# Kernel optimization log

Measured on AMD Instinct MI355X. Metric: run time of the kernel, lower is better.

Reference implementation:

```python
import jax, jax.numpy as jnp
import numpy as np

N, E, F, H, G = 50000, 600000, 128, 128, 256
EPS = 1e-5
NEG_SLOPE = 0.2


def setup_inputs() -> dict:
    key = jax.random.key(0)
    ks = jax.random.split(key, 20)
    def w(k, shape, fan_in):
        return jax.random.normal(k, shape, jnp.float32) / np.sqrt(fan_in)
    x = jax.random.normal(ks[0], (N, F), jnp.float32)
    edge_index = jax.random.randint(ks[1], (2, E), 0, N, jnp.int32)
    batch = jnp.sort(jax.random.randint(ks[2], (N,), 0, G, jnp.int32))
    return {
        "x": x, "edge_index": edge_index, "batch": batch,
        "W1": w(ks[3], (F, H), F), "b1": jnp.zeros((H,), jnp.float32),
        "g1": jnp.ones((H,), jnp.float32), "be1": jnp.zeros((H,), jnp.float32),
        "Wg": w(ks[4], (H, H), H), "att_src": w(ks[5], (H,), H),
        "att_dst": w(ks[6], (H,), H), "bg": jnp.zeros((H,), jnp.float32),
        "g2": jnp.ones((H,), jnp.float32), "be2": jnp.zeros((H,), jnp.float32),
        "W3": w(ks[7], (H, H), H), "b3": jnp.zeros((H,), jnp.float32),
        "g3": jnp.ones((H,), jnp.float32), "be3": jnp.zeros((H,), jnp.float32),
        "fw1": w(ks[8], (H, H), H), "fb1": jnp.zeros((H,), jnp.float32),
        "fw2": w(ks[9], (H, 1), H), "fb2": jnp.zeros((1,), jnp.float32),
    }


def _with_self_loops(edge_index):
    loop = jnp.arange(N, dtype=edge_index.dtype)
    src = jnp.concatenate([edge_index[0], loop])
    dst = jnp.concatenate([edge_index[1], loop])
    return src, dst


def gcn_conv(x, W, b, src, dst):
    h = x @ W                                      # [N,H]
    deg = jax.ops.segment_sum(jnp.ones_like(dst, jnp.float32), dst, num_segments=N)
    dis = jnp.where(deg > 0, jax.lax.rsqrt(jnp.maximum(deg, 1.0)), 0.0)
    norm = dis[src] * dis[dst]                     # [E+N]
    msg = h[src] * norm[:, None]
    return jax.ops.segment_sum(msg, dst, num_segments=N) + b


def gat_conv(x, W, a_src, a_dst, b, src, dst):
    # single-head PyG GATConv with self loops
    h = x @ W                                      # [N,H]
    al_s = h @ a_src                               # [N]
    al_d = h @ a_dst
    e = jax.nn.leaky_relu(al_s[src] + al_d[dst], NEG_SLOPE)   # [E+N]
    m = jax.ops.segment_max(e, dst, num_segments=N)
    ex = jnp.exp(e - m[dst])
    denom = jax.ops.segment_sum(ex, dst, num_segments=N)
    alpha = ex / denom[dst]
    out = jax.ops.segment_sum(h[src] * alpha[:, None], dst, num_segments=N)
    return out + b


def batch_norm(x, gamma, beta):
    mu = jnp.mean(x, axis=0)
    var = jnp.var(x, axis=0)
    return gamma * (x - mu) * jax.lax.rsqrt(var + EPS) + beta


def reference(x, edge_index, batch, W1, b1, g1, be1, Wg, att_src, att_dst, bg,
              g2, be2, W3, b3, g3, be3, fw1, fb1, fw2, fb2):
    src, dst = _with_self_loops(edge_index)
    h = jax.nn.relu(batch_norm(gcn_conv(x, W1, b1, src, dst), g1, be1))
    # dropout = identity (eval mode)
    h = jax.nn.relu(batch_norm(gat_conv(h, Wg, att_src, att_dst, bg, src, dst), g2, be2))
    h = jax.nn.relu(batch_norm(gcn_conv(h, W3, b3, src, dst), g3, be3))
    # global mean pool over graphs
    sums = jax.ops.segment_sum(h, batch, num_segments=G)           # [G,H]
    cnts = jax.ops.segment_sum(jnp.ones((h.shape[0],), h.dtype), batch, num_segments=G)
    pooled = sums / jnp.maximum(cnts, 1.0)[:, None]
    z = jax.nn.relu(pooled @ fw1 + fb1)
    return z @ fw2 + fb2                                            # [G,1]
```

## Files before the change

### kernel.cpp

```cpp
#include <hip/hip_runtime.h>
#include <hip/hip_fp16.h>
#include <cstdint>

#define N_NODES 50000
#define N_EDGES 600000
#define HDIM    128
#define NGRAPH  256
#define EPSBN   1e-5f
#define NEG     0.2f
#define SCAN_B  196

__device__ __forceinline__ float lrelu(float v){ return v > 0.f ? v : NEG*v; }

typedef _Float16 f16x8 __attribute__((ext_vector_type(8)));
typedef float    f32x4 __attribute__((ext_vector_type(4)));

__global__ void prep_kernel(const float* __restrict__ W1, const float* __restrict__ Wg,
                            const float* __restrict__ W3, __half* __restrict__ Wt1,
                            __half* __restrict__ Wtg, __half* __restrict__ Wt3,
                            const int* __restrict__ ei, int* __restrict__ degi,
                            const int* __restrict__ batch, int* __restrict__ start){
  int b = blockIdx.x;
  if (b < 192){
    const float* W = (b < 64) ? W1 : (b < 128 ? Wg : W3);
    __half*     Wt = (b < 64) ? Wt1 : (b < 128 ? Wtg : Wt3);
    int idx = (b & 63)*256 + threadIdx.x;
    int k = idx >> 7, n = idx & 127;
    Wt[n*128 + k] = __float2half(W[idx]);
  } else if (b < 192 + 2344){
    int e = (b - 192)*256 + threadIdx.x;
    if (e < N_EDGES) atomicAdd(&degi[ei[N_EDGES + e]], 1);
  } else {
    int i = (b - 192 - 2344)*256 + threadIdx.x;
    if (i >= N_NODES) return;
    int bb = batch[i];
    int p = (i == 0) ? -1 : batch[i-1];
    for (int g = p+1; g <= bb; ++g) start[g] = i;
    if (i == N_NODES-1)
      for (int g = bb+1; g <= NGRAPH; ++g) start[g] = N_NODES;
  }
}

template<bool BN, bool F32IN, bool ATT, bool SCALE>
__global__ __launch_bounds__(256) void gemm_mfma(const void* __restrict__ Xv,
    const __half* __restrict__ Wt, const __half* __restrict__ scH,
    const __half* __restrict__ shH, __half* __restrict__ Yh,
    const float* __restrict__ asr, const float* __restrict__ adt,
    float* __restrict__ al_s, float* __restrict__ al_d,
    const float* __restrict__ dis){
  const int t    = threadIdx.x;
  const int wave = t >> 6, lane = t & 63;
  const int q    = lane >> 4, c16 = lane & 15;
  const int m0   = blockIdx.x*64 + wave*16;
  const int row  = m0 + c16;
  const int arow = (row > N_NODES-1) ? N_NODES-1 : row;

  f32x4 acc[8];
#pragma unroll
  for (int i = 0; i < 8; ++i) acc[i] = (f32x4){0.f,0.f,0.f,0.f};

  const f16x8* Wt8 = (const f16x8*)Wt;

#pragma unroll
  for (int kc = 0; kc < 4; ++kc){
    const int kof = kc*32 + q*8;
    f16x8 a;
    if (F32IN){
      const float* xp = (const float*)Xv + (long)arow*128 + kof;
      float4 x0 = *(const float4*)xp;
      float4 x1 = *(const float4*)(xp + 4);
      a[0]=(_Float16)x0.x; a[1]=(_Float16)x0.y; a[2]=(_Float16)x0.z; a[3]=(_Float16)x0.w;
      a[4]=(_Float16)x1.x; a[5]=(_Float16)x1.y; a[6]=(_Float16)x1.z; a[7]=(_Float16)x1.w;
    } else {
      f16x8 raw = *(const f16x8*)((const _Float16*)Xv + (long)arow*128 + kof);
      if (BN){
        f16x8 scv = *(const f16x8*)((const _Float16*)scH + kof);
        f16x8 shv = *(const f16x8*)((const _Float16*)shH + kof);
#pragma unroll
        for (int i = 0; i < 8; ++i){
          _Float16 v = (_Float16)(raw[i]*scv[i] + shv[i]);
          a[i] = v > (_Float16)0 ? v : (_Float16)0;
        }
      } else {
        a = raw;
      }
    }
#pragma unroll
    for (int nt = 0; nt < 8; ++nt){
      f16x8 b = Wt8[(nt*16 + c16)*16 + kc*4 + q];
      acc[nt] = __builtin_amdgcn_mfma_f32_16x16x32_f16(b, a, acc[nt], 0, 0, 0);
    }
  }
  float rs = SCALE ? dis[arow] : 1.f;
  if (row < N_NODES){
    __half* yp = Yh + (long)row*128 + q*4;
#pragma unroll
    for (int nt = 0; nt < 8; ++nt){
      union { uint2 u; __half2 h[2]; } pk;
      pk.h[0] = __floats2half2_rn(acc[nt][0]*rs, acc[nt][1]*rs);
      pk.h[1] = __floats2half2_rn(acc[nt][2]*rs, acc[nt][3]*rs);
      *(uint2*)(yp + nt*16) = pk.u;
    }
  }
  if (ATT){
    float s = 0.f, d = 0.f;
#pragma unroll
    for (int nt = 0; nt < 8; ++nt){
      float4 av = *(const float4*)(asr + nt*16 + q*4);
      float4 bv = *(const float4*)(adt + nt*16 + q*4);
      s += acc[nt][0]*av.x + acc[nt][1]*av.y + acc[nt][2]*av.z + acc[nt][3]*av.w;
      d += acc[nt][0]*bv.x + acc[nt][1]*bv.y + acc[nt][2]*bv.z + acc[nt][3]*bv.w;
    }
    s += __shfl_xor(s, 16); s += __shfl_xor(s, 32);
    d += __shfl_xor(d, 16); d += __shfl_xor(d, 32);
    if (q == 0 && row < N_NODES){ al_s[row] = s; al_d[row] = d; }
  }
}

__global__ void scan_partial(const int* __restrict__ degi, int* __restrict__ part,
                             float* __restrict__ dis){
  __shared__ int sm[256];
  int t = threadIdx.x; int i = blockIdx.x*256 + t;
  int v = (i < N_NODES) ? degi[i] : 0;
  if (i < N_NODES) dis[i] = rsqrtf((float)v + 1.f);
  sm[t] = v;
  __syncthreads();
  for (int off = 128; off; off >>= 1){
    if (t < off) sm[t] += sm[t + off];
    __syncthreads();
  }
  if (t == 0) part[blockIdx.x] = sm[0];
}
__global__ void scan_offsets(int* part){
  __shared__ int sm[256];
  int t = threadIdx.x;
  int v = (t < SCAN_B) ? part[t] : 0;
  sm[t] = v; __syncthreads();
  for (int off = 1; off < 256; off <<= 1){
    int add = (t >= off) ? sm[t - off] : 0;
    __syncthreads();
    sm[t] += add; __syncthreads();
  }
  if (t < SCAN_B) part[t] = sm[t] - v;
}
__global__ void scan_final(const int* __restrict__ degi, const int* __restrict__ part,
                           int* __restrict__ rowp){
  __shared__ int sm[256];
  int t = threadIdx.x; int i = blockIdx.x*256 + t;
  int v = (i < N_NODES) ? degi[i] : 0;
  sm[t] = v; __syncthreads();
  for (int off = 1; off < 256; off <<= 1){
    int add = (t >= off) ? sm[t - off] : 0;
    __syncthreads();
    sm[t] += add; __syncthreads();
  }
  if (i < N_NODES) rowp[i] = part[blockIdx.x] + sm[t] - v;
}
__global__ void csr_scatter(const int* __restrict__ ei, const int* __restrict__ rowp,
                            int* __restrict__ fill, int* __restrict__ colx){
  int e = blockIdx.x*256 + threadIdx.x;
  if (e >= N_EDGES) return;
  int s = ei[e], d = ei[N_EDGES + e];
  int pos = rowp[d] + atomicAdd(&fill[d], 1);
  colx[pos] = s;
}

__global__ __launch_bounds__(256) void gcn_agg(const _Float16* __restrict__ Ah,
    const float* __restrict__ dis, const int* __restrict__ rowp,
    const int* __restrict__ degi, const int* __restrict__ colx,
    __half* __restrict__ Bh){
  const int n = blockIdx.x*4 + (threadIdx.x >> 6);
  const int lane = threadIdx.x & 63;
  const int g = lane >> 4, p = lane & 15;
  float acc[8] = {0,0,0,0,0,0,0,0};
  if (g == 0){
    f16x8 self = *(const f16x8*)(Ah + (long)n*128 + p*8);
#pragma unroll
    for (int i = 0; i < 8; ++i) acc[i] = (float)self[i];
  }
  const int e0 = rowp[n], cnt = degi[n];
  for (int base = 0; base < cnt; base += 64){
    int idx = base + lane;
    int s = 0; float w = 0.f;
    if (idx < cnt){ s = colx[e0 + idx]; w = 1.f; }
    int nit = min(64, cnt - base);
    int j = 0;
    for (; j + 8 <= nit; j += 8){
      int   s0 = __shfl(s, j + g),      s1 = __shfl(s, j + 4 + g);
      float w0 = __shfl(w, j + g),      w1 = __shfl(w, j + 4 + g);
      f16x8 r0 = *(const f16x8*)(Ah + (long)s0*128 + p*8);
      f16x8 r1 = *(const f16x8*)(Ah + (long)s1*128 + p*8);
#pragma unroll
      for (int i = 0; i < 8; ++i) acc[i] += w0 * (float)r0[i];
#pragma unroll
      for (int i = 0; i < 8; ++i) acc[i] += w1 * (float)r1[i];
    }
    for (; j < nit; j += 4){
      int   sj = __shfl(s, j + g);
      float wj = __shfl(w, j + g);
      f16x8 r = *(const f16x8*)(Ah + (long)sj*128 + p*8);
#pragma unroll
      for (int i = 0; i < 8; ++i) acc[i] += wj * (float)r[i];
    }
  }
#pragma unroll
  for (int i = 0; i < 8; ++i){
    acc[i] += __shfl_xor(acc[i], 16);
    acc[i] += __shfl_xor(acc[i], 32);
  }
  if (g == 0){
    float dn = dis[n];
    union { uint4 u; __half2 h[4]; } pk;
#pragma unroll
    for (int i = 0; i < 4; ++i)
      pk.h[i] = __floats2half2_rn(acc[2*i]*dn, acc[2*i+1]*dn);
    *(uint4*)(Bh + (long)n*128 + p*8) = pk.u;
  }
}

__global__ __launch_bounds__(256) void gat_agg(const _Float16* __restrict__ Ah,
    const float* __restrict__ al_s, const float* __restrict__ al_d,
    const int* __restrict__ rowp, const int* __restrict__ degi,
    const int* __restrict__ colx, __half* __restrict__ Bh){
  const int n = blockIdx.x*4 + (threadIdx.x >> 6);
  const int lane = threadIdx.x & 63;
  const int g = lane >> 4, p = lane & 15;
  const float adn = al_d[n];
  const float lself = lrelu(al_s[n] + adn);
  const int e0 = rowp[n], cnt = degi[n];
  int sReg = 0; float lv = -1e30f;
  if (lane < cnt){ sReg = colx[e0 + lane]; lv = lrelu(al_s[sReg] + adn); }
  float m = fmaxf(lself, lv);
  for (int base = 64; base < cnt; base += 64){
    int idx = base + lane;
    if (idx < cnt) m = fmaxf(m, lrelu(al_s[colx[e0 + idx]] + adn));
  }
#pragma unroll
  for (int off = 32; off; off >>= 1) m = fmaxf(m, __shfl_xor(m, off));
  const float exs = __expf(lself - m);
  float w = __expf(lv - m);
  float dpart = w;
  float acc[8] = {0,0,0,0,0,0,0,0};
  if (g == 0){
    f16x8 self = *(const f16x8*)(Ah + (long)n*128 + p*8);
#pragma unroll
    for (int i = 0; i < 8; ++i) acc[i] = exs * (float)self[i];
  }
  {
    int nit = min(64, cnt);
    int j = 0;
    for (; j + 8 <= nit; j += 8){
      int   s0 = __shfl(sReg, j + g),   s1 = __shfl(sReg, j + 4 + g);
      float w0 = __shfl(w,    j + g),   w1 = __shfl(w,    j + 4 + g);
      f16x8 r0 = *(const f16x8*)(Ah + (long)s0*128 + p*8);
      f16x8 r1 = *(const f16x8*)(Ah + (long)s1*128 + p*8);
#pragma unroll
      for (int i = 0; i < 8; ++i) acc[i] += w0 * (float)r0[i];
#pragma unroll
      for (int i = 0; i < 8; ++i) acc[i] += w1 * (float)r1[i];
    }
    for (; j < nit; j += 4){
      int   sj = __shfl(sReg, j + g);
      float wj = __shfl(w,    j + g);
      f16x8 r = *(const f16x8*)(Ah + (long)sj*128 + p*8);
#pragma unroll
      for (int i = 0; i < 8; ++i) acc[i] += wj * (float)r[i];
    }
  }
  for (int base = 64; base < cnt; base += 64){
    int idx = base + lane;
    int s2 = 0; float w2 = 0.f;
    if (idx < cnt){ s2 = colx[e0 + idx]; w2 = __expf(lrelu(al_s[s2] + adn) - m); }
    dpart += w2;
    int nit = min(64, cnt - base);
    for (int j = 0; j < nit; j += 4){
      int   sj = __shfl(s2, j + g);
      float wj = __shfl(w2, j + g);
      f16x8 r = *(const f16x8*)(Ah + (long)sj*128 + p*8);
#pragma unroll
      for (int i = 0; i < 8; ++i) acc[i] += wj * (float)r[i];
    }
  }
#pragma unroll
  for (int off = 32; off; off >>= 1) dpart += __shfl_xor(dpart, off);
#pragma unroll
  for (int i = 0; i < 8; ++i){
    acc[i] += __shfl_xor(acc[i], 16);
    acc[i] += __shfl_xor(acc[i], 32);
  }
  if (g == 0){
    float rinv = 1.f / (dpart + exs);
    union { uint4 u; __half2 h[4]; } pk;
#pragma unroll
    for (int i = 0; i < 4; ++i)
      pk.h[i] = __floats2half2_rn(acc[2*i]*rinv, acc[2*i+1]*rinv);
    *(uint4*)(Bh + (long)n*128 + p*8) = pk.u;
  }
}

__global__ void stats_h(const __half2* __restrict__ X2,
                        float* __restrict__ S, float* __restrict__ Q){
  __shared__ float s0m[256], s1m[256], q0m[256], q1m[256];
  int t = threadIdx.x;
  float s0=0,s1=0,q0=0,q1=0;
  int stride = gridDim.x*256;
  const int total = N_NODES*64;
  for (int idx = blockIdx.x*256 + t; idx < total; idx += stride){
    float2 f = __half22float2(X2[idx]);
    s0 += f.x; q0 += f.x*f.x; s1 += f.y; q1 += f.y*f.y;
  }
  s0m[t]=s0; s1m[t]=s1; q0m[t]=q0; q1m[t]=q1;
  __syncthreads();
  if (t < 64){
    float a0 = s0m[t]+s0m[t+64]+s0m[t+128]+s0m[t+192];
    float a1 = s1m[t]+s1m[t+64]+s1m[t+128]+s1m[t+192];
    float b0 = q0m[t]+q0m[t+64]+q0m[t+128]+q0m[t+192];
    float b1 = q1m[t]+q1m[t+64]+q1m[t+128]+q1m[t+192];
    atomicAdd(&S[2*t],   a0); atomicAdd(&S[2*t+1], a1);
    atomicAdd(&Q[2*t],   b0); atomicAdd(&Q[2*t+1], b1);
  }
}
__global__ void bnparam(const float* __restrict__ S, const float* __restrict__ Q,
                        const float* __restrict__ g, const float* __restrict__ be,
                        float* __restrict__ sc, float* __restrict__ sh,
                        __half* __restrict__ scH, __half* __restrict__ shH){
  int c = threadIdx.x;
  float mean = S[c] / (float)N_NODES;
  float var  = fmaxf(Q[c]/(float)N_NODES - mean*mean, 0.f);
  float scale = g[c]*rsqrtf(var + EPSBN);
  float shift = be[c] - mean*scale;
  sc[c] = scale;  sh[c] = shift;
  scH[c] = __float2half(scale);
  shH[c] = __float2half(shift);
}

__global__ void pool_h(const __half* __restrict__ Bh, const int* __restrict__ start,
                       const float* __restrict__ sc, const float* __restrict__ sh,
                       float* __restrict__ Pq){
  int g = blockIdx.x >> 2, q = blockIdx.x & 3, f = threadIdx.x;
  int s0 = start[g], len = start[g+1] - s0;
  int n0 = s0 + (len*q)/4, n1 = s0 + (len*(q+1))/4;
  float scl = sc[f], shf = sh[f];
  float acc = 0.f;
  for (int n = n0; n < n1; ++n)
    acc += fmaxf(__half2float(Bh[(long)n*128 + f])*scl + shf, 0.f);
  Pq[(long)blockIdx.x*128 + f] = acc;
}

__global__ void final_kernel(const float* __restrict__ Pq, const int* __restrict__ start,
                             const float* __restrict__ fw1, const float* __restrict__ fb1,
                             const float* __restrict__ fw2, const float* __restrict__ fb2,
                             float* __restrict__ out){
  __shared__ float p[128];
  __shared__ float red[2];
  int g = blockIdx.x, t = threadIdx.x;
  float cnt = fmaxf((float)(start[g+1] - start[g]), 1.f);
  float sum = Pq[(long)(g*4+0)*128+t] + Pq[(long)(g*4+1)*128+t]
            + Pq[(long)(g*4+2)*128+t] + Pq[(long)(g*4+3)*128+t];
  p[t] = sum / cnt;
  __syncthreads();
  float acc = fb1[t];
  for (int k = 0; k < 128; ++k) acc += p[k]*fw1[k*128 + t];
  float z = fmaxf(acc, 0.f) * fw2[t];
  for (int off = 32; off; off >>= 1) z += __shfl_down(z, off);
  if ((t & 63) == 0) red[t >> 6] = z;
  __syncthreads();
  if (t == 0) out[g] = red[0] + red[1] + fb2[0];
}

extern "C" void kernel_launch(void* const* d_in, const int* in_sizes, int n_in,
                              void* d_out, int out_size, void* d_ws, size_t ws_size,
                              hipStream_t stream){
  const float* x    = (const float*)d_in[0];
  const int*   ei   = (const int*)d_in[1];
  const int*   batch= (const int*)d_in[2];
  const float* W1   = (const float*)d_in[3];
  const float* g1   = (const float*)d_in[5];
  const float* be1  = (const float*)d_in[6];
  const float* Wg   = (const float*)d_in[7];
  const float* asr  = (const float*)d_in[8];
  const float* adt  = (const float*)d_in[9];
  const float* g2   = (const float*)d_in[11];
  const float* be2  = (const float*)d_in[12];
  const float* W3   = (const float*)d_in[13];
  const float* g3   = (const float*)d_in[15];
  const float* be3  = (const float*)d_in[16];
  const float* fw1  = (const float*)d_in[17];
  const float* fb1  = (const float*)d_in[18];
  const float* fw2  = (const float*)d_in[19];
  const float* fb2  = (const float*)d_in[20];
  float* out = (float*)d_out;

  const long NH = (long)N_NODES*HDIM;
  __half* Ah    = (__half*)d_ws;
  __half* Bh    = Ah + NH;
  __half* Wt1   = Bh + NH;
  __half* Wtg   = Wt1 + 16384;
  __half* Wt3   = Wtg + 16384;
  float* dis    = (float*)(Wt3 + 16384);
  float* al_s   = dis + N_NODES;
  float* al_d   = al_s + N_NODES;
  float* Pq     = al_d + N_NODES;
  float* sc     = Pq + (long)NGRAPH*4*HDIM;
  float* sh     = sc + HDIM;
  __half* scH   = (__half*)(sh + HDIM);
  __half* shH   = scH + HDIM;
  int* deg_i    = (int*)(shH + HDIM);
  int* fill     = deg_i + N_NODES;
  float* stats  = (float*)(fill + N_NODES);
  int* rowp     = (int*)(stats + 768);
  int* colx     = rowp + N_NODES;
  int* start    = colx + N_EDGES;
  int* part     = start + NGRAPH + 1;

  hipMemsetAsync(deg_i, 0, (size_t)(2*N_NODES + 768) * sizeof(int), stream);

  const int TB = 256;
  const int gE  = (N_EDGES + TB - 1)/TB;
  const int gMM = (N_NODES + 63)/64;
  const int gAgg= N_NODES / 4;

  const _Float16* Ahf = (const _Float16*)Ah;
  const __half2*  Bh2 = (const __half2*)Bh;

  prep_kernel<<<192 + gE + SCAN_B, TB, 0, stream>>>(W1, Wg, W3, Wt1, Wtg, Wt3,
                                                    ei, deg_i, batch, start);
  scan_partial<<<SCAN_B, TB, 0, stream>>>(deg_i, part, dis);
  scan_offsets<<<1, TB, 0, stream>>>(part);
  scan_final<<<SCAN_B, TB, 0, stream>>>(deg_i, part, rowp);
  csr_scatter<<<gE, TB, 0, stream>>>(ei, rowp, fill, colx);

  gemm_mfma<false,true,false,true><<<gMM, TB, 0, stream>>>(x, Wt1, nullptr, nullptr, Ah,
                                                 nullptr, nullptr, nullptr, nullptr, dis);
  gcn_agg<<<gAgg, TB, 0, stream>>>(Ahf, dis, rowp, deg_i, colx, Bh);
  stats_h<<<512, TB, 0, stream>>>(Bh2, stats + 0, stats + 128);
  bnparam<<<1, 128, 0, stream>>>(stats + 0, stats + 128, g1, be1, sc, sh, scH, shH);

  gemm_mfma<true,false,true,false><<<gMM, TB, 0, stream>>>(Bh, Wtg, scH, shH, Ah,
                                                 asr, adt, al_s, al_d, nullptr);
  gat_agg<<<gAgg, TB, 0, stream>>>(Ahf, al_s, al_d, rowp, deg_i, colx, Bh);
  stats_h<<<512, TB, 0, stream>>>(Bh2, stats + 256, stats + 384);
  bnparam<<<1, 128, 0, stream>>>(stats + 256, stats + 384, g2, be2, sc, sh, scH, shH);

  gemm_mfma<true,false,false,true><<<gMM, TB, 0, stream>>>(Bh, Wt3, scH, shH, Ah,
                                                 nullptr, nullptr, nullptr, nullptr, dis);
  gcn_agg<<<gAgg, TB, 0, stream>>>(Ahf, dis, rowp, deg_i, colx, Bh);
  stats_h<<<512, TB, 0, stream>>>(Bh2, stats + 512, stats + 640);
  bnparam<<<1, 128, 0, stream>>>(stats + 512, stats + 640, g3, be3, sc, sh, scH, shH);

  pool_h<<<NGRAPH*4, 128, 0, stream>>>(Bh, start, sc, sh, Pq);
  final_kernel<<<NGRAPH, 128, 0, stream>>>(Pq, start, fw1, fb1, fw2, fb2, out);
}
```

Before: 455.1 us.

## Fuse BN params into consumers, merge scan and pool kernels, repack weights

Folds the batch-norm parameter computation into the GEMM and the pooling kernel, which removes three bnparam launches. It merges scan_offsets into scan_final, with each block reducing the prefix of partial sums itself, and switches the CSR scatter to a single atomic cursor array. It also fuses pool and final MLP into one kernel, vectorizes stats_h to 8-wide loads, and repacks the transposed weights so MFMA B-loads are contiguous per lane. The aim is to cut launch count and small-kernel overhead, at the cost of redundant per-block BN and prefix recomputation.

```diff
diff --git a/kernel.cpp b/kernel.cpp
--- a/kernel.cpp
+++ b/kernel.cpp
@@ -26,7 +26,9 @@
     __half*     Wt = (b < 64) ? Wt1 : (b < 128 ? Wtg : Wt3);
     int idx = (b & 63)*256 + threadIdx.x;
     int k = idx >> 7, n = idx & 127;
-    Wt[n*128 + k] = __float2half(W[idx]);
+    int kc = k >> 5, q = (k >> 3) & 3, j = k & 7;
+    int nt = n >> 4, c16 = n & 15;
+    Wt[(((kc*8 + nt)*4 + q)*16 + c16)*8 + j] = __float2half(W[idx]);
   } else if (b < 192 + 2344){
     int e = (b - 192)*256 + threadIdx.x;
     if (e < N_EDGES) atomicAdd(&degi[ei[N_EDGES + e]], 1);
@@ -43,12 +45,26 @@
 
 template<bool BN, bool F32IN, bool ATT, bool SCALE>
 __global__ __launch_bounds__(256) void gemm_mfma(const void* __restrict__ Xv,
-    const __half* __restrict__ Wt, const __half* __restrict__ scH,
-    const __half* __restrict__ shH, __half* __restrict__ Yh,
+    const __half* __restrict__ Wt,
+    const float* __restrict__ S, const float* __restrict__ Q,
+    const float* __restrict__ gam, const float* __restrict__ bet,
+    __half* __restrict__ Yh,
     const float* __restrict__ asr, const float* __restrict__ adt,
     float* __restrict__ al_s, float* __restrict__ al_d,
     const float* __restrict__ dis){
+  __shared__ _Float16 scl[128], shl[128];
   const int t    = threadIdx.x;
+  if (BN){
+    if (t < 128){
+      float mean = S[t] * (1.f/(float)N_NODES);
+      float var  = fmaxf(Q[t]*(1.f/(float)N_NODES) - mean*mean, 0.f);
+      float scale = gam[t]*rsqrtf(var + EPSBN);
+      float shift = bet[t] - mean*scale;
+      scl[t] = (_Float16)scale;
+      shl[t] = (_Float16)shift;
+    }
+    __syncthreads();
+  }
   const int wave = t >> 6, lane = t & 63;
   const int q    = lane >> 4, c16 = lane & 15;
   const int m0   = blockIdx.x*64 + wave*16;
@@ -74,8 +90,8 @@
     } else {
       f16x8 raw = *(const f16x8*)((const _Float16*)Xv + (long)arow*128 + kof);
       if (BN){
-        f16x8 scv = *(const f16x8*)((const _Float16*)scH + kof);
-        f16x8 shv = *(const f16x8*)((const _Float16*)shH + kof);
+        f16x8 scv = *(const f16x8*)(scl + kof);
+        f16x8 shv = *(const f16x8*)(shl + kof);
 #pragma unroll
         for (int i = 0; i < 8; ++i){
           _Float16 v = (_Float16)(raw[i]*scv[i] + shv[i]);
@@ -87,7 +103,7 @@
     }
 #pragma unroll
     for (int nt = 0; nt < 8; ++nt){
-      f16x8 b = Wt8[(nt*16 + c16)*16 + kc*4 + q];
+      f16x8 b = Wt8[(kc*8 + nt)*64 + lane];
       acc[nt] = __builtin_amdgcn_mfma_f32_16x16x32_f16(b, a, acc[nt], 0, 0, 0);
     }
   }
@@ -131,22 +147,19 @@
   }
   if (t == 0) part[blockIdx.x] = sm[0];
 }
-__global__ void scan_offsets(int* part){
+__global__ void scan_final(const int* __restrict__ degi, const int* __restrict__ part,
+                           int* __restrict__ rowp, int* __restrict__ work){
   __shared__ int sm[256];
-  int t = threadIdx.x;
-  int v = (t < SCAN_B) ? part[t] : 0;
-  sm[t] = v; __syncthreads();
-  for (int off = 1; off < 256; off <<= 1){
-    int add = (t >= off) ? sm[t - off] : 0;
+  __shared__ int offs;
+  int t = threadIdx.x; int i = blockIdx.x*256 + t;
+  int pv = (t < SCAN_B && t < blockIdx.x) ? part[t] : 0;
+  sm[t] = pv; __syncthreads();
+  for (int off = 128; off; off >>= 1){
+    if (t < off) sm[t] += sm[t + off];
     __syncthreads();
-    sm[t] += add; __syncthreads();
-  }
-  if (t < SCAN_B) part[t] = sm[t] - v;
-}
-__global__ void scan_final(const int* __restrict__ degi, const int* __restrict__ part,
-                           int* __restrict__ rowp){
-  __shared__ int sm[256];
-  int t = threadIdx.x; int i = blockIdx.x*256 + t;
+  }
+  if (t == 0) offs = sm[0];
+  __syncthreads();
   int v = (i < N_NODES) ? degi[i] : 0;
   sm[t] = v; __syncthreads();
   for (int off = 1; off < 256; off <<= 1){
@@ -154,14 +167,18 @@
     __syncthreads();
     sm[t] += add; __syncthreads();
   }
-  if (i < N_NODES) rowp[i] = part[blockIdx.x] + sm[t] - v;
-}
-__global__ void csr_scatter(const int* __restrict__ ei, const int* __restrict__ rowp,
-                            int* __restrict__ fill, int* __restrict__ colx){
+  if (i < N_NODES){
+    int r = offs + sm[t] - v;
+    rowp[i] = r;
+    work[i] = r;
+  }
+}
+__global__ void csr_scatter(const int* __restrict__ ei, int* __restrict__ work,
+                            int* __restrict__ colx){
   int e = blockIdx.x*256 + threadIdx.x;
   if (e >= N_EDGES) return;
   int s = ei[e], d = ei[N_EDGES + e];
-  int pos = rowp[d] + atomicAdd(&fill[d], 1);
+  int pos = atomicAdd(&work[d], 1);
   colx[pos] = s;
 }
 
@@ -298,74 +315,72 @@
   }
 }
 
-__global__ void stats_h(const __half2* __restrict__ X2,
+__global__ void stats_h(const f16x8* __restrict__ X8,
                         float* __restrict__ S, float* __restrict__ Q){
-  __shared__ float s0m[256], s1m[256], q0m[256], q1m[256];
+  __shared__ float sb[16][16][8];
+  __shared__ float qb[16][16][8];
   int t = threadIdx.x;
-  float s0=0,s1=0,q0=0,q1=0;
-  int stride = gridDim.x*256;
-  const int total = N_NODES*64;
-  for (int idx = blockIdx.x*256 + t; idx < total; idx += stride){
-    float2 f = __half22float2(X2[idx]);
-    s0 += f.x; q0 += f.x*f.x; s1 += f.y; q1 += f.y*f.y;
-  }
-  s0m[t]=s0; s1m[t]=s1; q0m[t]=q0; q1m[t]=q1;
-  __syncthreads();
-  if (t < 64){
-    float a0 = s0m[t]+s0m[t+64]+s0m[t+128]+s0m[t+192];
-    float a1 = s1m[t]+s1m[t+64]+s1m[t+128]+s1m[t+192];
-    float b0 = q0m[t]+q0m[t+64]+q0m[t+128]+q0m[t+192];
-    float b1 = q1m[t]+q1m[t+64]+q1m[t+128]+q1m[t+192];
-    atomicAdd(&S[2*t],   a0); atomicAdd(&S[2*t+1], a1);
-    atomicAdd(&Q[2*t],   b0); atomicAdd(&Q[2*t+1], b1);
-  }
-}
-__global__ void bnparam(const float* __restrict__ S, const float* __restrict__ Q,
-                        const float* __restrict__ g, const float* __restrict__ be,
-                        float* __restrict__ sc, float* __restrict__ sh,
-                        __half* __restrict__ scH, __half* __restrict__ shH){
-  int c = threadIdx.x;
-  float mean = S[c] / (float)N_NODES;
-  float var  = fmaxf(Q[c]/(float)N_NODES - mean*mean, 0.f);
-  float scale = g[c]*rsqrtf(var + EPSBN);
-  float shift = be[c] - mean*scale;
-  sc[c] = scale;  sh[c] = shift;
-  scH[c] = __float2half(scale);
-  shH[c] = __float2half(shift);
-}
-
-__global__ void pool_h(const __half* __restrict__ Bh, const int* __restrict__ start,
-                       const float* __restrict__ sc, const float* __restrict__ sh,
-                       float* __restrict__ Pq){
-  int g = blockIdx.x >> 2, q = blockIdx.x & 3, f = threadIdx.x;
-  int s0 = start[g], len = start[g+1] - s0;
-  int n0 = s0 + (len*q)/4, n1 = s0 + (len*(q+1))/4;
-  float scl = sc[f], shf = sh[f];
+  int cg = t & 15, r = t >> 4;
+  float s[8] = {0,0,0,0,0,0,0,0}, q[8] = {0,0,0,0,0,0,0,0};
+  const int total = N_NODES*16;
+  for (int idx = blockIdx.x*256 + t; idx < total; idx += gridDim.x*256){
+    f16x8 v = X8[idx];
+#pragma unroll
+    for (int i = 0; i < 8; ++i){
+      float f = (float)v[i];
+      s[i] += f; q[i] += f*f;
+    }
+  }
+#pragma unroll
+  for (int i = 0; i < 8; ++i){ sb[r][cg][i] = s[i]; qb[r][cg][i] = q[i]; }
+  __syncthreads();
+  if (t < 128){
+    int cg2 = t >> 3, j = t & 7;
+    float as = 0.f, aq = 0.f;
+#pragma unroll
+    for (int r2 = 0; r2 < 16; ++r2){ as += sb[r2][cg2][j]; aq += qb[r2][cg2][j]; }
+    atomicAdd(&S[cg2*8 + j], as);
+    atomicAdd(&Q[cg2*8 + j], aq);
+  }
+}
+
+__global__ void poolfinal(const __half* __restrict__ Bh, const int* __restrict__ start,
+                          const float* __restrict__ S, const float* __restrict__ Q,
+                          const float* __restrict__ gam, const float* __restrict__ bet,
+                          const float* __restrict__ fw1, const float* __restrict__ fb1,
+                          const float* __restrict__ fw2, const float* __restrict__ fb2,
+                          float* __restrict__ out){
+  __shared__ float scl[128], shl[128], psum[2][128], p[128], red[2];
+  int t = threadIdx.x, gg = blockIdx.x;
+  if (t < 128){
+    float mean = S[t] * (1.f/(float)N_NODES);
+    float var  = fmaxf(Q[t]*(1.f/(float)N_NODES) - mean*mean, 0.f);
+    float scale = gam[t]*rsqrtf(var + EPSBN);
+    scl[t] = scale;
+    shl[t] = bet[t] - mean*scale;
+  }
+  __syncthreads();
+  int s0 = start[gg], s1 = start[gg+1];
+  int c = t & 127, h = t >> 7;
   float acc = 0.f;
-  for (int n = n0; n < n1; ++n)
-    acc += fmaxf(__half2float(Bh[(long)n*128 + f])*scl + shf, 0.f);
-  Pq[(long)blockIdx.x*128 + f] = acc;
-}
-
-__global__ void final_kernel(const float* __restrict__ Pq, const int* __restrict__ start,
-                             const float* __restrict__ fw1, const float* __restrict__ fb1,
-                             const float* __restrict__ fw2, const float* __restrict__ fb2,
-                             float* __restrict__ out){
-  __shared__ float p[128];
-  __shared__ float red[2];
-  int g = blockIdx.x, t = threadIdx.x;
-  float cnt = fmaxf((float)(start[g+1] - start[g]), 1.f);
-  float sum = Pq[(long)(g*4+0)*128+t] + Pq[(long)(g*4+1)*128+t]
-            + Pq[(long)(g*4+2)*128+t] + Pq[(long)(g*4+3)*128+t];
-  p[t] = sum / cnt;
-  __syncthreads();
-  float acc = fb1[t];
-  for (int k = 0; k < 128; ++k) acc += p[k]*fw1[k*128 + t];
-  float z = fmaxf(acc, 0.f) * fw2[t];
-  for (int off = 32; off; off >>= 1) z += __shfl_down(z, off);
-  if ((t & 63) == 0) red[t >> 6] = z;
-  __syncthreads();
-  if (t == 0) out[g] = red[0] + red[1] + fb2[0];
+  for (int n = s0 + h; n < s1; n += 2)
+    acc += fmaxf(__half2float(Bh[(long)n*128 + c])*scl[c] + shl[c], 0.f);
+  psum[h][c] = acc;
+  __syncthreads();
+  if (t < 128){
+    float cnt = fmaxf((float)(s1 - s0), 1.f);
+    p[t] = (psum[0][t] + psum[1][t]) / cnt;
+  }
+  __syncthreads();
+  if (t < 128){
+    float a = fb1[t];
+    for (int k = 0; k < 128; ++k) a += p[k]*fw1[k*128 + t];
+    float z = fmaxf(a, 0.f) * fw2[t];
+    for (int off = 32; off; off >>= 1) z += __shfl_down(z, off);
+    if ((t & 63) == 0) red[t >> 6] = z;
+  }
+  __syncthreads();
+  if (t == 0) out[gg] = red[0] + red[1] + fb2[0];
 }
 
 extern "C" void kernel_launch(void* const* d_in, const int* in_sizes, int n_in,
@@ -400,20 +415,15 @@
   float* dis    = (float*)(Wt3 + 16384);
   float* al_s   = dis + N_NODES;
   float* al_d   = al_s + N_NODES;
-  float* Pq     = al_d + N_NODES;
-  float* sc     = Pq + (long)NGRAPH*4*HDIM;
-  float* sh     = sc + HDIM;
-  __half* scH   = (__half*)(sh + HDIM);
-  __half* shH   = scH + HDIM;
-  int* deg_i    = (int*)(shH + HDIM);
-  int* fill     = deg_i + N_NODES;
-  float* stats  = (float*)(fill + N_NODES);
+  int* deg_i    = (int*)(al_d + N_NODES);
+  float* stats  = (float*)(deg_i + N_NODES);
   int* rowp     = (int*)(stats + 768);
-  int* colx     = rowp + N_NODES;
+  int* work     = rowp + N_NODES;
+  int* colx     = work + N_NODES;
   int* start    = colx + N_EDGES;
   int* part     = start + NGRAPH + 1;
 
-  hipMemsetAsync(deg_i, 0, (size_t)(2*N_NODES + 768) * sizeof(int), stream);
+  hipMemsetAsync(deg_i, 0, (size_t)(N_NODES + 768) * sizeof(int), stream);
 
   const int TB = 256;
   const int gE  = (N_EDGES + TB - 1)/TB;
@@ -421,33 +431,29 @@
   const int gAgg= N_NODES / 4;
 
   const _Float16* Ahf = (const _Float16*)Ah;
-  const __half2*  Bh2 = (const __half2*)Bh;
+  const f16x8*    Bh8 = (const f16x8*)Bh;
 
   prep_kernel<<<192 + gE + SCAN_B, TB, 0, stream>>>(W1, Wg, W3, Wt1, Wtg, Wt3,
                                                     ei, deg_i, batch, start);
   scan_partial<<<SCAN_B, TB, 0, stream>>>(deg_i, part, dis);
-  scan_offsets<<<1, TB, 0, stream>>>(part);
-  scan_final<<<SCAN_B, TB, 0, stream>>>(deg_i, part, rowp);
-  csr_scatter<<<gE, TB, 0, stream>>>(ei, rowp, fill, colx);
-
-  gemm_mfma<false,true,false,true><<<gMM, TB, 0, stream>>>(x, Wt1, nullptr, nullptr, Ah,
-                                                 nullptr, nullptr, nullptr, nullptr, dis);
+  scan_final<<<SCAN_B, TB, 0, stream>>>(deg_i, part, rowp, work);
+  csr_scatter<<<gE, TB, 0, stream>>>(ei, work, colx);
+
+  gemm_mfma<false,true,false,true><<<gMM, TB, 0, stream>>>(x, Wt1,
+      nullptr, nullptr, nullptr, nullptr, Ah, nullptr, nullptr, nullptr, nullptr, dis);
   gcn_agg<<<gAgg, TB, 0, stream>>>(Ahf, dis, rowp, deg_i, colx, Bh);
-  stats_h<<<512, TB, 0, stream>>>(Bh2, stats + 0, stats + 128);
-  bnparam<<<1, 128, 0, stream>>>(stats + 0, stats + 128, g1, be1, sc, sh, scH, shH);
-
-  gemm_mfma<true,false,true,false><<<gMM, TB, 0, stream>>>(Bh, Wtg, scH, shH, Ah,
-                                                 asr, adt, al_s, al_d, nullptr);
+  stats_h<<<512, TB, 0, stream>>>(Bh8, stats + 0, stats + 128);
+
+  gemm_mfma<true,false,true,false><<<gMM, TB, 0, stream>>>(Bh, Wtg,
+      stats + 0, stats + 128, g1, be1, Ah, asr, adt, al_s, al_d, nullptr);
   gat_agg<<<gAgg, TB, 0, stream>>>(Ahf, al_s, al_d, rowp, deg_i, colx, Bh);
-  stats_h<<<512, TB, 0, stream>>>(Bh2, stats + 256, stats + 384);
-  bnparam<<<1, 128, 0, stream>>>(stats + 256, stats + 384, g2, be2, sc, sh, scH, shH);
-
-  gemm_mfma<true,false,false,true><<<gMM, TB, 0, stream>>>(Bh, Wt3, scH, shH, Ah,
-                                                 nullptr, nullptr, nullptr, nullptr, dis);
+  stats_h<<<512, TB, 0, stream>>>(Bh8, stats + 256, stats + 384);
+
+  gemm_mfma<true,false,false,true><<<gMM, TB, 0, stream>>>(Bh, Wt3,
+      stats + 256, stats + 384, g2, be2, Ah, nullptr, nullptr, nullptr, nullptr, dis);
   gcn_agg<<<gAgg, TB, 0, stream>>>(Ahf, dis, rowp, deg_i, colx, Bh);
-  stats_h<<<512, TB, 0, stream>>>(Bh2, stats + 512, stats + 640);
-  bnparam<<<1, 128, 0, stream>>>(stats + 512, stats + 640, g3, be3, sc, sh, scH, shH);
-
-  pool_h<<<NGRAPH*4, 128, 0, stream>>>(Bh, start, sc, sh, Pq);
-  final_kernel<<<NGRAPH, 128, 0, stream>>>(Pq, start, fw1, fb1, fw2, fb2, out);
-}
+  stats_h<<<512, TB, 0, stream>>>(Bh8, stats + 512, stats + 640);
+
+  poolfinal<<<NGRAPH, TB, 0, stream>>>(Bh, start, stats + 512, stats + 640, g3, be3,
+                                       fw1, fb1, fw2, fb2, out);
+}
```

Measured after the change: 377.9 us. 1.2x faster.
